# Optimization experiments

Measured on AMD Instinct MI355X. Metric: run time of the kernel, lower is better.

## Reference

```python
import jax, jax.numpy as jnp
import numpy as np

D_MODEL = 1024
MAX_NUM_LAYERS = 4


def setup_inputs() -> dict:
    key = jax.random.key(0)
    ks = jax.random.split(key, 8)
    S, B, D, L = 1024, 2, D_MODEL, 3
    w = lambda k: (jax.random.normal(k, (D, D), dtype=jnp.float32) * 0.02)
    return {
        "x": jax.random.normal(ks[0], (S, B, D), dtype=jnp.float32),
        "layer_outputs": jax.random.normal(ks[1], (L, S, B, D), dtype=jnp.float32),
        "Wq": w(ks[2]), "bq": jnp.zeros((D,), jnp.float32),
        "Wk": w(ks[3]), "bk": jnp.zeros((D,), jnp.float32),
        "Wv": w(ks[4]), "bv": jnp.zeros((D,), jnp.float32),
        "Wo": w(ks[5]), "bo": jnp.zeros((D,), jnp.float32),
        "layer_weights": jnp.ones((MAX_NUM_LAYERS + 1,), jnp.float32),
        "num_heads": 16,
    }


def reference(x, layer_outputs, Wq, bq, Wk, bk, Wv, bv, Wo, bo, layer_weights, num_heads):
    # x: [S, B, D]; layer_outputs: [L, S, B, D] (stacked prev layer outputs)
    S, B, D = x.shape
    H = num_heads
    hd = D // H
    scale = hd ** -0.5
    # q from x only: [S, B*H, hd] -> [BH, S, hd]
    q = (x @ Wq.T + bq).reshape(S, B * H, hd).transpose(1, 0, 2)
    # k/v from x and all previous layer outputs (shared K/V projections)
    xs = jnp.concatenate([x[None], layer_outputs], axis=0)          # [Lp1, S, B, D]
    Lp1 = xs.shape[0]
    k = (xs @ Wk.T + bk).reshape(Lp1, S, B * H, hd).transpose(0, 2, 1, 3)  # [Lp1, BH, S, hd]
    v = (xs @ Wv.T + bv).reshape(Lp1, S, B * H, hd).transpose(0, 2, 1, 3)
    # per-layer scores, softmax over the key axis (torch dim=-2 of stacked scores)
    scores = jnp.einsum('bqd,lbkd->lbqk', q, k) * scale             # [Lp1, BH, S, S]
    attn = jax.nn.softmax(scores, axis=-1)
    lw = jax.nn.softmax(layer_weights[:Lp1])                        # [Lp1]
    combined = jnp.einsum('l,lbqk,lbkd->bqd', lw, attn, v)          # [BH, S, hd]
    combined = combined.transpose(1, 0, 2).reshape(S, B, D)
    return combined @ Wo.T + bo
```

## Files before the change

kernel.cpp:

```cpp
#include <hip/hip_runtime.h>
#include <hip/hip_bf16.h>
#include <math.h>

#define S_LEN   1024
#define BATCH   2
#define DMODEL  1024
#define NHEADS  16
#define HDIM    64
#define BHEADS  32
#define LP1     4
#define ROWS_PL 2048

typedef __attribute__((ext_vector_type(8)))  short bf16x8;
typedef __attribute__((ext_vector_type(4)))  float f32x4;
typedef __attribute__((ext_vector_type(16))) float f32x16;

__device__ inline ushort bf16_rne(float a) {
    unsigned u = __float_as_uint(a);
    return (ushort)((u + 0x7FFFu + ((u >> 16) & 1u)) >> 16);
}
__device__ inline float bf16_up(ushort h) { return __uint_as_float(((unsigned)h) << 16); }
__device__ inline void split_bf16(float a, ushort &hi, ushort &lo) {
    hi = bf16_rne(a);
    lo = bf16_rne(a - bf16_up(hi));
}
__device__ inline uint pk_bf16(float a, float b) {
    float2 f; f.x = a; f.y = b;
    __hip_bfloat162 h = __float22bfloat162_rn(f);
    return *reinterpret_cast<uint*>(&h);
}
#if __has_builtin(__builtin_amdgcn_exp2f)
__device__ inline float fast_exp2(float x) { return __builtin_amdgcn_exp2f(x); }
#else
__device__ inline float fast_exp2(float x) { return exp2f(x); }
#endif

__device__ inline void permswap(uint &a, uint &b) {
    asm("v_permlane32_swap_b32 %0, %1" : "+v"(a), "+v"(b));
}

__device__ inline void glds16(const ushort* g, ushort* l) {
    __builtin_amdgcn_global_load_lds(
        (const __attribute__((address_space(1))) void*)g,
        (__attribute__((address_space(3))) void*)l, 16, 0, 0);
}

#define SCLF 0.18033688011112042f

__global__ __launch_bounds__(256)
void presplit(const float* __restrict__ x, const float* __restrict__ lo,
              const float* __restrict__ Wq, const float* __restrict__ Wk,
              const float* __restrict__ Wv, const float* __restrict__ Wo,
              ushort* __restrict__ XsH, ushort* __restrict__ WH,
              ushort* __restrict__ WL)
{
    const int z = blockIdx.z;
    const float* src; ushort* dh; ushort* dl = nullptr; int n;
    if (z == 0)      { src = x;  dh = XsH;           n = 2097152; }
    else if (z == 1) { src = lo; dh = XsH + 2097152; n = 6291456; }
    else {
        const float* wsrc[4] = { Wq, Wk, Wv, Wo };
        src = wsrc[z - 2];
        dh = WH + (size_t)(z - 2) * 1048576;
        if (z == 2 || z == 5) dl = WL + (size_t)(z - 2) * 1048576;
        n = 1048576;
    }
    const int i = (blockIdx.x * 256 + threadIdx.x) * 8;
    if (i >= n) return;
    float v[8];
    *(float4*)&v[0] = *(const float4*)(src + i);
    *(float4*)&v[4] = *(const float4*)(src + i + 4);
    ushort h[8];
    #pragma unroll
    for (int j = 0; j < 8; ++j) h[j] = bf16_rne(v[j]);
    *(uint4*)(dh + i) = *(uint4*)h;
    if (dl) {
        ushort l[8];
        #pragma unroll
        for (int j = 0; j < 8; ++j) l[j] = bf16_rne(v[j] - bf16_up(h[j]));
        *(uint4*)(dl + i) = *(uint4*)l;
    }
}

template<int MODE>
__global__ __launch_bounds__(256)
void proj_g(const ushort* __restrict__ Abf,
            const ushort* __restrict__ Bhg, const ushort* __restrict__ Blg,
            const float* __restrict__ bias,
            float* __restrict__ outf, ushort* __restrict__ outh,
            ushort* __restrict__ outl)
{
    __shared__ ushort smem[2][3 * 2048];

    const int fid = blockIdx.x;
    const int nt = (fid & 7) * 2 + ((fid >> 3) & 1);
    const int mt = fid >> 4;
    const int m0 = mt * 64, n0 = nt * 64;

    const int t  = threadIdx.x;
    const int wv = t >> 6, lane = t & 63;
    const int quad = lane >> 4, r = lane & 15;
    const int wm = wv & 1, wn = wv >> 1;
    const int mBase = wm * 32, nBase = wn * 32;

    const int lrow = lane >> 2;
    const int lch  = ((lane & 3) ^ (lrow & 3)) * 8;
    const ushort* Asrc  = Abf + (size_t)(m0 + wv * 16 + lrow) * DMODEL + lch;
    const ushort* Bhsrc = Bhg + (size_t)(n0 + wv * 16 + lrow) * DMODEL + lch;
    const ushort* Blsrc = Blg + (size_t)(n0 + wv * 16 + lrow) * DMODEL + lch;

    const int q0x = (quad ^ (r & 3)) << 3;
    f32x4 acc[2][2];
    #pragma unroll
    for (int i = 0; i < 2; ++i)
        #pragma unroll
        for (int j = 0; j < 2; ++j) acc[i][j] = (f32x4){0.f, 0.f, 0.f, 0.f};

    glds16(Asrc,  smem[0]        + wv * 512);
    glds16(Bhsrc, smem[0] + 2048 + wv * 512);
    glds16(Blsrc, smem[0] + 4096 + wv * 512);

    for (int k = 0; k < 32; ++k) {
        const int cur = k & 1;
        __syncthreads();
        if (k + 1 < 32) {
            const int off = (k + 1) * 32;
            glds16(Asrc  + off, smem[cur ^ 1]        + wv * 512);
            glds16(Bhsrc + off, smem[cur ^ 1] + 2048 + wv * 512);
            glds16(Blsrc + off, smem[cur ^ 1] + 4096 + wv * 512);
        }
        const ushort* Ah = smem[cur];
        const ushort* Bh = smem[cur] + 2048;
        const ushort* Bl = smem[cur] + 4096;
        bf16x8 fa[2], fbh[2], fbl[2];
        #pragma unroll
        for (int i = 0; i < 2; ++i)
            fa[i] = *(const bf16x8*)&Ah[(mBase + i * 16 + r) * 32 + q0x];
        #pragma unroll
        for (int j = 0; j < 2; ++j) {
            fbh[j] = *(const bf16x8*)&Bh[(nBase + j * 16 + r) * 32 + q0x];
            fbl[j] = *(const bf16x8*)&Bl[(nBase + j * 16 + r) * 32 + q0x];
        }
        #pragma unroll
        for (int i = 0; i < 2; ++i)
            #pragma unroll
            for (int j = 0; j < 2; ++j) {
                acc[i][j] = __builtin_amdgcn_mfma_f32_16x16x32_bf16(fa[i], fbh[j], acc[i][j], 0, 0, 0);
                acc[i][j] = __builtin_amdgcn_mfma_f32_16x16x32_bf16(fa[i], fbl[j], acc[i][j], 0, 0, 0);
            }
    }

    const int cn = lane & 15;
    #pragma unroll
    for (int j = 0; j < 2; ++j) {
        const int n = n0 + nBase + j * 16 + cn;
        const float bv = bias[n];
        #pragma unroll
        for (int i = 0; i < 2; ++i) {
            const int mrow = m0 + mBase + i * 16 + quad * 4;
            #pragma unroll
            for (int g = 0; g < 4; ++g) {
                const int m = mrow + g;
                if (MODE == 1) {
                    outf[(size_t)m * DMODEL + n] = acc[i][j][g] + bv;
                } else {
                    const float val = (acc[i][j][g] + bv) * SCLF;
                    const int s = m >> 1, b = m & 1;
                    const int bh = b * 16 + (n >> 6), e = n & 63;
                    const size_t idx = (((size_t)bh * S_LEN) + s) * HDIM + e;
                    ushort hi, lov; split_bf16(val, hi, lov);
                    outh[idx] = hi; outl[idx] = lov;
                }
            }
        }
    }
}

__global__ __launch_bounds__(256, 4)
void proj_kv(const ushort* __restrict__ XsH,
             const ushort* __restrict__ KWh, const ushort* __restrict__ VWh,
             const float* __restrict__ bk, const float* __restrict__ bv,
             ushort* __restrict__ kout, ushort* __restrict__ vout)
{
    __shared__ ushort smem[2][10240];

    const int t  = threadIdx.x;
    const int m0 = blockIdx.y * 64, n0 = blockIdx.x * 128;
    const int lyr = m0 >> 11;

    const int wv = t >> 6, lane = t & 63;
    const int quad = lane >> 4, r = lane & 15;
    const int wm = wv & 1, wn = wv >> 1;
    const int mBase = wm * 32, nBase = wn * 64;

    const int lrow = lane >> 2;
    const int lch  = ((lane & 3) ^ (lrow & 3)) * 8;

    const ushort* Asrc = XsH + (size_t)(m0 + wv * 16 + lrow) * DMODEL + lch;
    const ushort* Bw[2] = { KWh, VWh };
    const ushort* Bsrc[2][2];
    #pragma unroll
    for (int p = 0; p < 2; ++p)
        #pragma unroll
        for (int seg = 0; seg < 2; ++seg)
            Bsrc[p][seg] = Bw[p] + (size_t)(n0 + wv * 32 + seg * 16 + lrow) * DMODEL + lch;

    const int q0x = (quad ^ (r & 3)) << 3;

    f32x4 aK[2][4], aV[2][4];
    #pragma unroll
    for (int i = 0; i < 2; ++i)
        #pragma unroll
        for (int j = 0; j < 4; ++j) {
            aK[i][j] = (f32x4){0.f, 0.f, 0.f, 0.f};
            aV[i][j] = (f32x4){0.f, 0.f, 0.f, 0.f};
        }

    glds16(Asrc, smem[0] + wv * 512);
    #pragma unroll
    for (int p = 0; p < 2; ++p)
        #pragma unroll
        for (int seg = 0; seg < 2; ++seg)
            glds16(Bsrc[p][seg], smem[0] + 2048 + p * 4096 + (wv * 2 + seg) * 512);

    for (int k = 0; k < 32; ++k) {
        const int cur = k & 1;
        __syncthreads();
        if (k + 1 < 32) {
            const int off = (k + 1) * 32;
            glds16(Asrc + off, smem[cur ^ 1] + wv * 512);
            #pragma unroll
            for (int p = 0; p < 2; ++p)
                #pragma unroll
                for (int seg = 0; seg < 2; ++seg)
                    glds16(Bsrc[p][seg] + off,
                           smem[cur ^ 1] + 2048 + p * 4096 + (wv * 2 + seg) * 512);
        }
        const ushort* Ah = smem[cur];
        const ushort* Bp = smem[cur] + 2048;

        bf16x8 fa[2];
        #pragma unroll
        for (int i = 0; i < 2; ++i)
            fa[i] = *(const bf16x8*)&Ah[(mBase + i * 16 + r) * 32 + q0x];
        #pragma unroll
        for (int j = 0; j < 4; ++j) {
            const int off = (nBase + j * 16 + r) * 32 + q0x;
            const bf16x8 fkh = *(const bf16x8*)&Bp[off];
            const bf16x8 fvh = *(const bf16x8*)&Bp[4096 + off];
            #pragma unroll
            for (int i = 0; i < 2; ++i) {
                aK[i][j] = __builtin_amdgcn_mfma_f32_16x16x32_bf16(fa[i], fkh, aK[i][j], 0, 0, 0);
                aV[i][j] = __builtin_amdgcn_mfma_f32_16x16x32_bf16(fa[i], fvh, aV[i][j], 0, 0, 0);
            }
        }
    }

    const int cn = lane & 15;

    #pragma unroll
    for (int j = 0; j < 4; ++j) {
        const int n = n0 + nBase + j * 16 + cn;
        const float bb = bk[n];
        const int e    = n & 63;
        const int es_k = e >> 4, half_k = (e >> 3) & 1, j_k = e & 7;
        const int h    = n >> 6;
        #pragma unroll
        for (int i = 0; i < 2; ++i) {
            #pragma unroll
            for (int g = 0; g < 4; ++g) {
                const int m = m0 + mBase + i * 16 + quad * 4 + g;
                const int rem = m & 2047, s = rem >> 1, b = rem & 1;
                const int bhI = lyr * 32 + b * 16 + h;
                const int kt  = s >> 5;
                const int lnk = half_k * 32 + (s & 31);
                kout[(size_t)bhI * 65536 + (size_t)(kt * 4 + es_k) * 512 + lnk * 8 + j_k]
                    = bf16_rne(aK[i][j][g] + bb);
            }
        }
    }

    ushort* T = smem[0];
    __syncthreads();
    #pragma unroll
    for (int j = 0; j < 4; ++j) {
        const int nloc = nBase + j * 16 + cn;
        const float bb = bv[n0 + nloc];
        #pragma unroll
        for (int i = 0; i < 2; ++i) {
            #pragma unroll
            for (int g = 0; g < 4; ++g) {
                const int mloc = mBase + i * 16 + quad * 4 + g;
                T[nloc * 66 + mloc] = bf16_rne(aV[i][j][g] + bb);
            }
        }
    }
    __syncthreads();
    {
        const int nloc = t >> 1, bsel = t & 1;
        const int n = n0 + nloc, h = n >> 6;
        const int e = n & 63;
        const int dg = e >> 5, lid_v = e & 31;
        const int s0g = (m0 & 2047) >> 1;
        const int kt  = s0g >> 5;
        const int bhI = lyr * 32 + bsel * 16 + h;
        ushort* dstb = vout + (size_t)bhI * 65536 + (size_t)kt * 2048;
        #pragma unroll
        for (int c = 0; c < 4; ++c) {
            ushort tmp[8];
            #pragma unroll
            for (int j = 0; j < 8; ++j)
                tmp[j] = T[nloc * 66 + 2 * (c * 8 + j) + bsel];
            const int ks = c >> 1, hv = c & 1;
            *(uint4*)(dstb + (ks * 2 + dg) * 512 + (hv * 32 + lid_v) * 8) = *(uint4*)tmp;
        }
    }
}

__global__ __launch_bounds__(256, 2)
void attn_mfma(const ushort* __restrict__ qhg, const ushort* __restrict__ qlg,
               const ushort* __restrict__ kh, const ushort* __restrict__ vth,
               const float* __restrict__ lwraw, float* __restrict__ part)
{
    const int t    = threadIdx.x;
    const int wv   = t >> 6, lane = t & 63;
    const int half = lane >> 5, lid = lane & 31;

    const int fid  = blockIdx.x;
    const int xcd  = fid & 7, slot = fid >> 3;
    const int pair = xcd * 16 + (slot >> 2);
    const int qt   = slot & 3;
    const int bh   = pair & 31, l = pair >> 5;
    const int qbase = qt * 256 + wv * 64;

    float wl;
    {
        float v[LP1], wm = -3.0e38f;
        #pragma unroll
        for (int i = 0; i < LP1; ++i) { v[i] = lwraw[i]; wm = fmaxf(wm, v[i]); }
        float ws = 0.f;
        #pragma unroll
        for (int i = 0; i < LP1; ++i) { v[i] = __expf(v[i] - wm); ws += v[i]; }
        wl = v[l] / ws;
    }

    bf16x8 qh[2][4], ql[2][4];
    #pragma unroll
    for (int u = 0; u < 2; ++u) {
        const size_t qoff = ((size_t)bh * S_LEN + qbase + u * 32 + lid) * HDIM + half * 8;
        #pragma unroll
        for (int es = 0; es < 4; ++es) {
            qh[u][es] = *(const bf16x8*)(qhg + qoff + es * 16);
            ql[u][es] = *(const bf16x8*)(qlg + qoff + es * 16);
        }
    }

    f32x16 o[2][2];
    #pragma unroll
    for (int u = 0; u < 2; ++u)
        #pragma unroll
        for (int dg = 0; dg < 2; ++dg)
            #pragma unroll
            for (int i = 0; i < 16; ++i) o[u][dg][i] = 0.f;
    float ls[2] = {0.f, 0.f};

    f32x16 zf;
    #pragma unroll
    for (int i = 0; i < 16; ++i) zf[i] = 0.f;

    const size_t kvo = (size_t)(l * BHEADS + bh) * S_LEN * HDIM;
    const ushort* kfb = kh  + kvo + (size_t)lane * 8;
    const ushort* vfb = vth + kvo + (size_t)lane * 8;

    bf16x8 kb[4], kn[4];
    #pragma unroll
    for (int es = 0; es < 4; ++es)
        kb[es] = *(const bf16x8*)(kfb + es * 512);
    #pragma unroll
    for (int es = 0; es < 4; ++es)
        kn[es] = *(const bf16x8*)(kfb + 2048 + es * 512);

    f32x16 sa[2];
    #pragma unroll
    for (int es = 0; es < 4; ++es)
        #pragma unroll
        for (int u = 0; u < 2; ++u) {
            sa[u] = __builtin_amdgcn_mfma_f32_32x32x16_bf16(kb[es], qh[u][es],
                                                            es == 0 ? zf : sa[u], 0, 0, 0);
            sa[u] = __builtin_amdgcn_mfma_f32_32x32x16_bf16(kb[es], ql[u][es], sa[u], 0, 0, 0);
        }

    for (int kt = 0; kt < 32; ++kt) {
        bf16x8 vb[2][2];
        {
            const ushort* vp = vfb + (size_t)kt * 2048;
            #pragma unroll
            for (int ks = 0; ks < 2; ++ks)
                #pragma unroll
                for (int dg = 0; dg < 2; ++dg)
                    vb[ks][dg] = *(const bf16x8*)(vp + (ks * 2 + dg) * 512);
        }

        bf16x8 pf[2][2];
        #pragma unroll
        for (int ks = 0; ks < 2; ++ks) {
            #pragma unroll
            for (int u = 0; u < 2; ++u) {
                const float p0 = fast_exp2(sa[u][8 * ks + 0]);
                const float p1 = fast_exp2(sa[u][8 * ks + 1]);
                const float p2 = fast_exp2(sa[u][8 * ks + 2]);
                const float p3 = fast_exp2(sa[u][8 * ks + 3]);
                const float p4 = fast_exp2(sa[u][8 * ks + 4]);
                const float p5 = fast_exp2(sa[u][8 * ks + 5]);
                const float p6 = fast_exp2(sa[u][8 * ks + 6]);
                const float p7 = fast_exp2(sa[u][8 * ks + 7]);
                ls[u] += ((p0 + p1) + (p2 + p3)) + ((p4 + p5) + (p6 + p7));

                uint a0 = pk_bf16(p0, p1);
                uint a1 = pk_bf16(p2, p3);
                uint b0 = pk_bf16(p4, p5);
                uint b1 = pk_bf16(p6, p7);
                permswap(a0, b0);
                permswap(a1, b1);
                union { uint w[4]; bf16x8 v; } pu;
                pu.w[0] = a0; pu.w[1] = a1; pu.w[2] = b0; pu.w[3] = b1;
                pf[ks][u] = pu.v;
            }
        }

        #pragma unroll
        for (int es = 0; es < 4; ++es) kb[es] = kn[es];
        {
            const ushort* kp = kfb + (size_t)((kt + 2) & 31) * 2048;
            #pragma unroll
            for (int es = 0; es < 4; ++es) kn[es] = *(const bf16x8*)(kp + es * 512);
        }

        __builtin_amdgcn_s_setprio(1);
        #pragma unroll
        for (int es = 0; es < 4; ++es)
            #pragma unroll
            for (int u = 0; u < 2; ++u) {
                sa[u] = __builtin_amdgcn_mfma_f32_32x32x16_bf16(kb[es], qh[u][es],
                                                                es == 0 ? zf : sa[u], 0, 0, 0);
                sa[u] = __builtin_amdgcn_mfma_f32_32x32x16_bf16(kb[es], ql[u][es], sa[u], 0, 0, 0);
            }
        __builtin_amdgcn_s_setprio(0);

        __builtin_amdgcn_s_setprio(1);
        #pragma unroll
        for (int ks = 0; ks < 2; ++ks)
            #pragma unroll
            for (int dg = 0; dg < 2; ++dg)
                #pragma unroll
                for (int u = 0; u < 2; ++u)
                    o[u][dg] = __builtin_amdgcn_mfma_f32_32x32x16_bf16(vb[ks][dg], pf[ks][u], o[u][dg], 0, 0, 0);
        __builtin_amdgcn_s_setprio(0);
    }

    const int b = bh >> 4, hh = bh & 15;
    #pragma unroll
    for (int u = 0; u < 2; ++u) {
        float lsv = ls[u];
        lsv += __shfl_xor(lsv, 32);
        const float sc = wl / lsv;
        const int q = qbase + u * 32 + lid;
        float* pb = part + (size_t)l * (ROWS_PL * DMODEL)
                  + ((size_t)q * BATCH + b) * DMODEL + hh * HDIM;
        #pragma unroll
        for (int dg = 0; dg < 2; ++dg)
            #pragma unroll
            for (int rq = 0; rq < 4; ++rq) {
                float4 vv;
                vv.x = o[u][dg][rq * 4 + 0] * sc;
                vv.y = o[u][dg][rq * 4 + 1] * sc;
                vv.z = o[u][dg][rq * 4 + 2] * sc;
                vv.w = o[u][dg][rq * 4 + 3] * sc;
                *(float4*)(pb + dg * 32 + rq * 8 + half * 4) = vv;
            }
    }
}

__global__ __launch_bounds__(256)
void sum_y(const float* __restrict__ part, ushort* __restrict__ YH)
{
    const int i = (blockIdx.x * 256 + threadIdx.x) * 8;
    float acc[8];
    #pragma unroll
    for (int c = 0; c < 2; ++c) {
        float4 s = *(const float4*)(part + i + c * 4);
        #pragma unroll
        for (int l = 1; l < LP1; ++l) {
            const float4 p = *(const float4*)(part + (size_t)l * 2097152 + i + c * 4);
            s.x += p.x; s.y += p.y; s.z += p.z; s.w += p.w;
        }
        acc[c * 4 + 0] = s.x; acc[c * 4 + 1] = s.y;
        acc[c * 4 + 2] = s.z; acc[c * 4 + 3] = s.w;
    }
    uint out[4];
    #pragma unroll
    for (int c = 0; c < 4; ++c) out[c] = pk_bf16(acc[c * 2], acc[c * 2 + 1]);
    *(uint4*)(YH + i) = *(uint4*)out;
}

extern "C" void kernel_launch(void* const* d_in, const int* in_sizes, int n_in,
                              void* d_out, int out_size, void* d_ws, size_t ws_size,
                              hipStream_t stream) {
    const float* x  = (const float*)d_in[0];
    const float* lo = (const float*)d_in[1];
    const float* Wq = (const float*)d_in[2];
    const float* bq = (const float*)d_in[3];
    const float* Wk = (const float*)d_in[4];
    const float* bk = (const float*)d_in[5];
    const float* Wv = (const float*)d_in[6];
    const float* bv = (const float*)d_in[7];
    const float* Wo = (const float*)d_in[8];
    const float* bo = (const float*)d_in[9];
    const float* lw = (const float*)d_in[10];
    float* out = (float*)d_out;

    char* ws = (char*)d_ws;
    ushort* XsH  = (ushort*)(ws);
    ushort* WH   = (ushort*)(ws + 16777216);
    ushort* WL   = (ushort*)(ws + 25165824);
    ushort* qhb  = (ushort*)(ws + 33554432);
    ushort* qlb  = (ushort*)(ws + 37748736);
    ushort* khb  = (ushort*)(ws + 41943040);
    ushort* vthb = (ushort*)(ws + 58720256);
    float*  part = (float*)(ws + 75497472);
    ushort* YH   = (ushort*)(ws + 109051904);

    dim3 blk(256);
    presplit<<<dim3(3072, 1, 6), blk, 0, stream>>>(x, lo, Wq, Wk, Wv, Wo, XsH, WH, WL);
    proj_g<0><<<dim3(512), blk, 0, stream>>>(XsH, WH, WL, bq, nullptr, qhb, qlb);
    proj_kv<<<dim3(8, 128), blk, 0, stream>>>(XsH,
        WH + 1048576, WH + 2097152, bk, bv, khb, vthb);
    attn_mfma<<<dim3(512), blk, 0, stream>>>(qhb, qlb, khb, vthb, lw, part);
    sum_y<<<dim3(1024), blk, 0, stream>>>(part, YH);
    proj_g<1><<<dim3(512), blk, 0, stream>>>(YH, WH + 3145728, WL + 3145728, bo, out, nullptr, nullptr);
}
```

Measured before the change: 248.4 us.

## Fuse Q and KV projections into one interleaved launch with larger KV tiles

Merges the Q projection and the K/V projection into a single kernel whose odd blocks compute Q tiles and even blocks compute K/V tiles, removing one launch and letting both GEMMs share the GPU at the same time. The KV tiles grow from 64x128 to 128x128 per block, which doubles reuse of each loaded weight tile and halves the KV block count. The cost is more accumulator registers per thread (launch bounds drop to 2 blocks per CU), more shared memory per block, and a possible load imbalance because Q blocks and KV blocks do different amounts of work.

```diff
diff --git a/kernel.cpp b/kernel.cpp
--- a/kernel.cpp
+++ b/kernel.cpp
@@ -82,13 +82,234 @@
     }
 }
 
-template<int MODE>
+__global__ __launch_bounds__(256, 2)
+void proj_qkv(const ushort* __restrict__ XsH,
+              const ushort* __restrict__ WH, const ushort* __restrict__ WL,
+              const float* __restrict__ bq, const float* __restrict__ bk,
+              const float* __restrict__ bv,
+              ushort* __restrict__ qhb, ushort* __restrict__ qlb,
+              ushort* __restrict__ kout, ushort* __restrict__ vout)
+{
+    __shared__ ushort smem[2][12288];
+    const int bid = blockIdx.x;
+    const int t   = threadIdx.x;
+    const int wv  = t >> 6, lane = t & 63;
+    const int quad = lane >> 4, r = lane & 15;
+    const int lrow = lane >> 2;
+    const int lch  = ((lane & 3) ^ (lrow & 3)) * 8;
+    const int q0x  = (quad ^ (r & 3)) << 3;
+    const int cn   = lane & 15;
+
+    if (bid & 1) {
+        const int fid = bid >> 1;
+        const int nt = (fid & 7) * 2 + ((fid >> 3) & 1);
+        const int mt = fid >> 4;
+        const int m0 = mt * 64, n0 = nt * 64;
+
+        const int wm = wv & 1, wn = wv >> 1;
+        const int mBase = wm * 32, nBase = wn * 32;
+
+        const ushort* Asrc  = XsH + (size_t)(m0 + wv * 16 + lrow) * DMODEL + lch;
+        const ushort* Bhsrc = WH  + (size_t)(n0 + wv * 16 + lrow) * DMODEL + lch;
+        const ushort* Blsrc = WL  + (size_t)(n0 + wv * 16 + lrow) * DMODEL + lch;
+
+        f32x4 acc[2][2];
+        #pragma unroll
+        for (int i = 0; i < 2; ++i)
+            #pragma unroll
+            for (int j = 0; j < 2; ++j) acc[i][j] = (f32x4){0.f, 0.f, 0.f, 0.f};
+
+        glds16(Asrc,  smem[0]        + wv * 512);
+        glds16(Bhsrc, smem[0] + 2048 + wv * 512);
+        glds16(Blsrc, smem[0] + 4096 + wv * 512);
+
+        for (int k = 0; k < 32; ++k) {
+            const int cur = k & 1;
+            __syncthreads();
+            if (k + 1 < 32) {
+                const int off = (k + 1) * 32;
+                glds16(Asrc  + off, smem[cur ^ 1]        + wv * 512);
+                glds16(Bhsrc + off, smem[cur ^ 1] + 2048 + wv * 512);
+                glds16(Blsrc + off, smem[cur ^ 1] + 4096 + wv * 512);
+            }
+            const ushort* Ah = smem[cur];
+            const ushort* Bh = smem[cur] + 2048;
+            const ushort* Bl = smem[cur] + 4096;
+            bf16x8 fa[2], fbh[2], fbl[2];
+            #pragma unroll
+            for (int i = 0; i < 2; ++i)
+                fa[i] = *(const bf16x8*)&Ah[(mBase + i * 16 + r) * 32 + q0x];
+            #pragma unroll
+            for (int j = 0; j < 2; ++j) {
+                fbh[j] = *(const bf16x8*)&Bh[(nBase + j * 16 + r) * 32 + q0x];
+                fbl[j] = *(const bf16x8*)&Bl[(nBase + j * 16 + r) * 32 + q0x];
+            }
+            #pragma unroll
+            for (int i = 0; i < 2; ++i)
+                #pragma unroll
+                for (int j = 0; j < 2; ++j) {
+                    acc[i][j] = __builtin_amdgcn_mfma_f32_16x16x32_bf16(fa[i], fbh[j], acc[i][j], 0, 0, 0);
+                    acc[i][j] = __builtin_amdgcn_mfma_f32_16x16x32_bf16(fa[i], fbl[j], acc[i][j], 0, 0, 0);
+                }
+        }
+
+        #pragma unroll
+        for (int j = 0; j < 2; ++j) {
+            const int n = n0 + nBase + j * 16 + cn;
+            const float bvv = bq[n];
+            #pragma unroll
+            for (int i = 0; i < 2; ++i) {
+                const int mrow = m0 + mBase + i * 16 + quad * 4;
+                #pragma unroll
+                for (int g = 0; g < 4; ++g) {
+                    const int m = mrow + g;
+                    const float val = (acc[i][j][g] + bvv) * SCLF;
+                    const int s = m >> 1, b = m & 1;
+                    const int bh = b * 16 + (n >> 6), e = n & 63;
+                    const size_t idx = (((size_t)bh * S_LEN) + s) * HDIM + e;
+                    ushort hi, lov; split_bf16(val, hi, lov);
+                    qhb[idx] = hi; qlb[idx] = lov;
+                }
+            }
+        }
+    } else {
+        const int fid = bid >> 1;
+        const int n0 = (fid & 7) * 128;
+        const int m0 = (fid >> 3) * 128;
+        const int lyr = m0 >> 11;
+
+        const int wm = wv & 1, wn = wv >> 1;
+        const int mBase = wm * 64, nBase = wn * 64;
+
+        const ushort* KWh = WH + 1048576;
+        const ushort* VWh = WH + 2097152;
+        const ushort* Asrc0 = XsH + (size_t)(m0 + wv * 16 + lrow) * DMODEL + lch;
+        const ushort* Asrc1 = Asrc0 + (size_t)64 * DMODEL;
+        const ushort* Bw[2] = { KWh, VWh };
+        const ushort* Bsrc[2][2];
+        #pragma unroll
+        for (int p = 0; p < 2; ++p)
+            #pragma unroll
+            for (int seg = 0; seg < 2; ++seg)
+                Bsrc[p][seg] = Bw[p] + (size_t)(n0 + wv * 32 + seg * 16 + lrow) * DMODEL + lch;
+
+        f32x4 aK[4][4], aV[4][4];
+        #pragma unroll
+        for (int i = 0; i < 4; ++i)
+            #pragma unroll
+            for (int j = 0; j < 4; ++j) {
+                aK[i][j] = (f32x4){0.f, 0.f, 0.f, 0.f};
+                aV[i][j] = (f32x4){0.f, 0.f, 0.f, 0.f};
+            }
+
+        glds16(Asrc0, smem[0]        + wv * 512);
+        glds16(Asrc1, smem[0] + 2048 + wv * 512);
+        #pragma unroll
+        for (int p = 0; p < 2; ++p)
+            #pragma unroll
+            for (int seg = 0; seg < 2; ++seg)
+                glds16(Bsrc[p][seg], smem[0] + 4096 + p * 4096 + (wv * 2 + seg) * 512);
+
+        for (int k = 0; k < 32; ++k) {
+            const int cur = k & 1;
+            __syncthreads();
+            if (k + 1 < 32) {
+                const int off = (k + 1) * 32;
+                glds16(Asrc0 + off, smem[cur ^ 1]        + wv * 512);
+                glds16(Asrc1 + off, smem[cur ^ 1] + 2048 + wv * 512);
+                #pragma unroll
+                for (int p = 0; p < 2; ++p)
+                    #pragma unroll
+                    for (int seg = 0; seg < 2; ++seg)
+                        glds16(Bsrc[p][seg] + off,
+                               smem[cur ^ 1] + 4096 + p * 4096 + (wv * 2 + seg) * 512);
+            }
+            const ushort* Ah = smem[cur];
+            const ushort* Bp = smem[cur] + 4096;
+
+            bf16x8 fa[4];
+            #pragma unroll
+            for (int i = 0; i < 4; ++i)
+                fa[i] = *(const bf16x8*)&Ah[(mBase + i * 16 + r) * 32 + q0x];
+            #pragma unroll
+            for (int j = 0; j < 4; ++j) {
+                const int off2 = (nBase + j * 16 + r) * 32 + q0x;
+                const bf16x8 fkh = *(const bf16x8*)&Bp[off2];
+                const bf16x8 fvh = *(const bf16x8*)&Bp[4096 + off2];
+                #pragma unroll
+                for (int i = 0; i < 4; ++i) {
+                    aK[i][j] = __builtin_amdgcn_mfma_f32_16x16x32_bf16(fa[i], fkh, aK[i][j], 0, 0, 0);
+                    aV[i][j] = __builtin_amdgcn_mfma_f32_16x16x32_bf16(fa[i], fvh, aV[i][j], 0, 0, 0);
+                }
+            }
+        }
+
+        #pragma unroll
+        for (int j = 0; j < 4; ++j) {
+            const int n = n0 + nBase + j * 16 + cn;
+            const float bb = bk[n];
+            const int e    = n & 63;
+            const int es_k = e >> 4, half_k = (e >> 3) & 1, j_k = e & 7;
+            const int h    = n >> 6;
+            #pragma unroll
+            for (int i = 0; i < 4; ++i) {
+                #pragma unroll
+                for (int g = 0; g < 4; ++g) {
+                    const int m = m0 + mBase + i * 16 + quad * 4 + g;
+                    const int rem = m & 2047, s = rem >> 1, b = rem & 1;
+                    const int bhI = lyr * 32 + b * 16 + h;
+                    const int kt  = s >> 5;
+                    const int lnk = half_k * 32 + (s & 31);
+                    kout[(size_t)bhI * 65536 + (size_t)(kt * 4 + es_k) * 512 + lnk * 8 + j_k]
+                        = bf16_rne(aK[i][j][g] + bb);
+                }
+            }
+        }
+
+        ushort* T = &smem[0][0];
+        __syncthreads();
+        #pragma unroll
+        for (int j = 0; j < 4; ++j) {
+            const int nloc = nBase + j * 16 + cn;
+            const float bb = bv[n0 + nloc];
+            #pragma unroll
+            for (int i = 0; i < 4; ++i) {
+                #pragma unroll
+                for (int g = 0; g < 4; ++g) {
+                    const int mloc = mBase + i * 16 + quad * 4 + g;
+                    T[nloc * 130 + mloc] = bf16_rne(aV[i][j][g] + bb);
+                }
+            }
+        }
+        __syncthreads();
+        {
+            const int nloc = t >> 1, bsel = t & 1;
+            const int n = n0 + nloc, h = n >> 6;
+            const int e = n & 63;
+            const int dg = e >> 5, lid_v = e & 31;
+            const int s0g = (m0 & 2047) >> 1;
+            const int kt0 = s0g >> 5;
+            const int bhI = lyr * 32 + bsel * 16 + h;
+            #pragma unroll
+            for (int c = 0; c < 8; ++c) {
+                ushort tmp[8];
+                #pragma unroll
+                for (int j = 0; j < 8; ++j)
+                    tmp[j] = T[nloc * 130 + 2 * (c * 8 + j) + bsel];
+                const int kt = kt0 + (c >> 2);
+                const int c2 = c & 3;
+                const int ks = c2 >> 1, hv = c2 & 1;
+                ushort* dstb = vout + (size_t)bhI * 65536 + (size_t)kt * 2048;
+                *(uint4*)(dstb + (ks * 2 + dg) * 512 + (hv * 32 + lid_v) * 8) = *(uint4*)tmp;
+            }
+        }
+    }
+}
+
 __global__ __launch_bounds__(256)
-void proj_g(const ushort* __restrict__ Abf,
+void proj_o(const ushort* __restrict__ Abf,
             const ushort* __restrict__ Bhg, const ushort* __restrict__ Blg,
-            const float* __restrict__ bias,
-            float* __restrict__ outf, ushort* __restrict__ outh,
-            ushort* __restrict__ outl)
+            const float* __restrict__ bias, float* __restrict__ outf)
 {
     __shared__ ushort smem[2][3 * 2048];
 
@@ -154,165 +375,13 @@
     #pragma unroll
     for (int j = 0; j < 2; ++j) {
         const int n = n0 + nBase + j * 16 + cn;
-        const float bv = bias[n];
+        const float bvv = bias[n];
         #pragma unroll
         for (int i = 0; i < 2; ++i) {
             const int mrow = m0 + mBase + i * 16 + quad * 4;
             #pragma unroll
-            for (int g = 0; g < 4; ++g) {
-                const int m = mrow + g;
-                if (MODE == 1) {
-                    outf[(size_t)m * DMODEL + n] = acc[i][j][g] + bv;
-                } else {
-                    const float val = (acc[i][j][g] + bv) * SCLF;
-                    const int s = m >> 1, b = m & 1;
-                    const int bh = b * 16 + (n >> 6), e = n & 63;
-                    const size_t idx = (((size_t)bh * S_LEN) + s) * HDIM + e;
-                    ushort hi, lov; split_bf16(val, hi, lov);
-                    outh[idx] = hi; outl[idx] = lov;
-                }
-            }
-        }
-    }
-}
-
-__global__ __launch_bounds__(256, 4)
-void proj_kv(const ushort* __restrict__ XsH,
-             const ushort* __restrict__ KWh, const ushort* __restrict__ VWh,
-             const float* __restrict__ bk, const float* __restrict__ bv,
-             ushort* __restrict__ kout, ushort* __restrict__ vout)
-{
-    __shared__ ushort smem[2][10240];
-
-    const int t  = threadIdx.x;
-    const int m0 = blockIdx.y * 64, n0 = blockIdx.x * 128;
-    const int lyr = m0 >> 11;
-
-    const int wv = t >> 6, lane = t & 63;
-    const int quad = lane >> 4, r = lane & 15;
-    const int wm = wv & 1, wn = wv >> 1;
-    const int mBase = wm * 32, nBase = wn * 64;
-
-    const int lrow = lane >> 2;
-    const int lch  = ((lane & 3) ^ (lrow & 3)) * 8;
-
-    const ushort* Asrc = XsH + (size_t)(m0 + wv * 16 + lrow) * DMODEL + lch;
-    const ushort* Bw[2] = { KWh, VWh };
-    const ushort* Bsrc[2][2];
-    #pragma unroll
-    for (int p = 0; p < 2; ++p)
-        #pragma unroll
-        for (int seg = 0; seg < 2; ++seg)
-            Bsrc[p][seg] = Bw[p] + (size_t)(n0 + wv * 32 + seg * 16 + lrow) * DMODEL + lch;
-
-    const int q0x = (quad ^ (r & 3)) << 3;
-
-    f32x4 aK[2][4], aV[2][4];
-    #pragma unroll
-    for (int i = 0; i < 2; ++i)
-        #pragma unroll
-        for (int j = 0; j < 4; ++j) {
-            aK[i][j] = (f32x4){0.f, 0.f, 0.f, 0.f};
-            aV[i][j] = (f32x4){0.f, 0.f, 0.f, 0.f};
-        }
-
-    glds16(Asrc, smem[0] + wv * 512);
-    #pragma unroll
-    for (int p = 0; p < 2; ++p)
-        #pragma unroll
-        for (int seg = 0; seg < 2; ++seg)
-            glds16(Bsrc[p][seg], smem[0] + 2048 + p * 4096 + (wv * 2 + seg) * 512);
-
-    for (int k = 0; k < 32; ++k) {
-        const int cur = k & 1;
-        __syncthreads();
-        if (k + 1 < 32) {
-            const int off = (k + 1) * 32;
-            glds16(Asrc + off, smem[cur ^ 1] + wv * 512);
-            #pragma unroll
-            for (int p = 0; p < 2; ++p)
-                #pragma unroll
-                for (int seg = 0; seg < 2; ++seg)
-                    glds16(Bsrc[p][seg] + off,
-                           smem[cur ^ 1] + 2048 + p * 4096 + (wv * 2 + seg) * 512);
-        }
-        const ushort* Ah = smem[cur];
-        const ushort* Bp = smem[cur] + 2048;
-
-        bf16x8 fa[2];
-        #pragma unroll
-        for (int i = 0; i < 2; ++i)
-            fa[i] = *(const bf16x8*)&Ah[(mBase + i * 16 + r) * 32 + q0x];
-        #pragma unroll
-        for (int j = 0; j < 4; ++j) {
-            const int off = (nBase + j * 16 + r) * 32 + q0x;
-            const bf16x8 fkh = *(const bf16x8*)&Bp[off];
-            const bf16x8 fvh = *(const bf16x8*)&Bp[4096 + off];
-            #pragma unroll
-            for (int i = 0; i < 2; ++i) {
-                aK[i][j] = __builtin_amdgcn_mfma_f32_16x16x32_bf16(fa[i], fkh, aK[i][j], 0, 0, 0);
-                aV[i][j] = __builtin_amdgcn_mfma_f32_16x16x32_bf16(fa[i], fvh, aV[i][j], 0, 0, 0);
-            }
-        }
-    }
-
-    const int cn = lane & 15;
-
-    #pragma unroll
-    for (int j = 0; j < 4; ++j) {
-        const int n = n0 + nBase + j * 16 + cn;
-        const float bb = bk[n];
-        const int e    = n & 63;
-        const int es_k = e >> 4, half_k = (e >> 3) & 1, j_k = e & 7;
-        const int h    = n >> 6;
-        #pragma unroll
-        for (int i = 0; i < 2; ++i) {
-            #pragma unroll
-            for (int g = 0; g < 4; ++g) {
-                const int m = m0 + mBase + i * 16 + quad * 4 + g;
-                const int rem = m & 2047, s = rem >> 1, b = rem & 1;
-                const int bhI = lyr * 32 + b * 16 + h;
-                const int kt  = s >> 5;
-                const int lnk = half_k * 32 + (s & 31);
-                kout[(size_t)bhI * 65536 + (size_t)(kt * 4 + es_k) * 512 + lnk * 8 + j_k]
-                    = bf16_rne(aK[i][j][g] + bb);
-            }
-        }
-    }
-
-    ushort* T = smem[0];
-    __syncthreads();
-    #pragma unroll
-    for (int j = 0; j < 4; ++j) {
-        const int nloc = nBase + j * 16 + cn;
-        const float bb = bv[n0 + nloc];
-        #pragma unroll
-        for (int i = 0; i < 2; ++i) {
-            #pragma unroll
-            for (int g = 0; g < 4; ++g) {
-                const int mloc = mBase + i * 16 + quad * 4 + g;
-                T[nloc * 66 + mloc] = bf16_rne(aV[i][j][g] + bb);
-            }
-        }
-    }
-    __syncthreads();
-    {
-        const int nloc = t >> 1, bsel = t & 1;
-        const int n = n0 + nloc, h = n >> 6;
-        const int e = n & 63;
-        const int dg = e >> 5, lid_v = e & 31;
-        const int s0g = (m0 & 2047) >> 1;
-        const int kt  = s0g >> 5;
-        const int bhI = lyr * 32 + bsel * 16 + h;
-        ushort* dstb = vout + (size_t)bhI * 65536 + (size_t)kt * 2048;
-        #pragma unroll
-        for (int c = 0; c < 4; ++c) {
-            ushort tmp[8];
-            #pragma unroll
-            for (int j = 0; j < 8; ++j)
-                tmp[j] = T[nloc * 66 + 2 * (c * 8 + j) + bsel];
-            const int ks = c >> 1, hv = c & 1;
-            *(uint4*)(dstb + (ks * 2 + dg) * 512 + (hv * 32 + lid_v) * 8) = *(uint4*)tmp;
+            for (int g = 0; g < 4; ++g)
+                outf[(size_t)(mrow + g) * DMODEL + n] = acc[i][j][g] + bvv;
         }
     }
 }
@@ -532,10 +601,9 @@
 
     dim3 blk(256);
     presplit<<<dim3(3072, 1, 6), blk, 0, stream>>>(x, lo, Wq, Wk, Wv, Wo, XsH, WH, WL);
-    proj_g<0><<<dim3(512), blk, 0, stream>>>(XsH, WH, WL, bq, nullptr, qhb, qlb);
-    proj_kv<<<dim3(8, 128), blk, 0, stream>>>(XsH,
-        WH + 1048576, WH + 2097152, bk, bv, khb, vthb);
+    proj_qkv<<<dim3(1024), blk, 0, stream>>>(XsH, WH, WL, bq, bk, bv,
+                                             qhb, qlb, khb, vthb);
     attn_mfma<<<dim3(512), blk, 0, stream>>>(qhb, qlb, khb, vthb, lw, part);
     sum_y<<<dim3(1024), blk, 0, stream>>>(part, YH);
-    proj_g<1><<<dim3(512), blk, 0, stream>>>(YH, WH + 3145728, WL + 3145728, bo, out, nullptr, nullptr);
-}
+    proj_o<<<dim3(512), blk, 0, stream>>>(YH, WH + 3145728, WL + 3145728, bo, out);
+}
```

Result: no change. 247.2 us (-0.5%).
